# Kernel optimization log

Hardware: AMD Instinct MI355X
Metric: run time of the kernel (lower is better)

Reference implementation:

```python
import jax, jax.numpy as jnp
import numpy as np

HEADS = 12
D_HEAD = 64  # d_model // heads


def _split_heads(t, heads, d_head):
    # Faithful to the torch code: transpose(1,2) -> (B, C, T), then
    # reshape (B, -1, heads, d_head), then transpose(1,2) -> (B, heads, T', d_head).
    B = t.shape[0]
    t = jnp.swapaxes(t, 1, 2)                      # (B, C, T)
    t = t.reshape(B, -1, heads, d_head)            # (B, T', heads, d_head) -- layout quirk preserved
    return jnp.swapaxes(t, 1, 2)                   # (B, heads, T', d_head)


def setup_inputs() -> dict:
    key = jax.random.key(0)
    ks = jax.random.split(key, 10)
    B, Tq, Tkv, D = 8, 4096, 77, 768
    s = 0.02
    return {
        "x": jax.random.normal(ks[0], (B, Tq, D), jnp.float32),
        "prompt": jax.random.normal(ks[1], (B, Tkv, D), jnp.float32),
        "Wq": jax.random.normal(ks[2], (D, D), jnp.float32) * s,
        "bq": jax.random.normal(ks[3], (D,), jnp.float32) * s,
        "Wk": jax.random.normal(ks[4], (D, D), jnp.float32) * s,
        "bk": jax.random.normal(ks[5], (D,), jnp.float32) * s,
        "Wv": jax.random.normal(ks[6], (D, D), jnp.float32) * s,
        "bv": jax.random.normal(ks[7], (D,), jnp.float32) * s,
        "Wp": jax.random.normal(ks[8], (D, D), jnp.float32) * s,
        "bp": jax.random.normal(ks[9], (D,), jnp.float32) * s,
    }


def reference(x, prompt, Wq, bq, Wk, bk, Wv, bv, Wp, bp):
    B, Tq, C = x.shape
    Ckv = prompt.shape[-1]
    q = _split_heads(x @ Wq.T + bq, HEADS, D_HEAD)       # (B, H, Tq, d_head)
    k = _split_heads(prompt @ Wk.T + bk, HEADS, D_HEAD)  # (B, H, Tkv, d_head)
    v = _split_heads(prompt @ Wv.T + bv, HEADS, D_HEAD)
    scale = 1.0 / jnp.sqrt(jnp.asarray(Ckv, x.dtype))    # note: sqrt(d_prompt), as in source
    att = jnp.einsum('bhqd,bhkd->bhqk', q, k) * scale
    att = jax.nn.softmax(att, axis=-1)
    out = jnp.einsum('bhqk,bhkd->bhqd', att, v)          # (B, H, Tq, d_head)
    out = jnp.swapaxes(out, 1, 2).reshape(B, Tq, C)
    return out @ Wp.T + bp                               # dropout = identity (eval)
```

## Files before the change

kernel.cpp:

```cpp
#include <hip/hip_runtime.h>

typedef __attribute__((ext_vector_type(8))) __bf16 bf16x8;
typedef __attribute__((ext_vector_type(4))) float f32x4;
typedef __attribute__((ext_vector_type(8))) unsigned short u16x8;
typedef __attribute__((ext_vector_type(4))) unsigned short u16x4;

#define DEV __device__ __forceinline__

DEV float bf2f(unsigned short u) {
  unsigned int x = ((unsigned int)u) << 16;
  return __builtin_bit_cast(float, x);
}
DEV unsigned short f2bf(float f) {
  unsigned int u = __builtin_bit_cast(unsigned int, f);
  u = u + 0x7fffu + ((u >> 16) & 1u);
  return (unsigned short)(u >> 16);
}
DEV unsigned int cvtpk(float a, float b) {
  unsigned int r;
  asm("v_cvt_pk_bf16_f32 %0, %1, %2" : "=v"(r) : "v"(a), "v"(b));
  return r;
}

DEV void glds16(const void* g, void* l) {
  __builtin_amdgcn_global_load_lds(
      (__attribute__((address_space(1))) void*)g,
      (__attribute__((address_space(3))) void*)l, 16, 0, 0);
}

__global__ __launch_bounds__(256) void k_prep(
    const float* __restrict__ x, const float* __restrict__ Wq,
    const float* __restrict__ Wk, const float* __restrict__ Wv,
    const float* __restrict__ Wp, const float* __restrict__ prompt,
    const float* __restrict__ bk, const float* __restrict__ bv,
    unsigned short* __restrict__ xb, unsigned short* __restrict__ wqb,
    unsigned short* __restrict__ wkvb, unsigned short* __restrict__ wpb,
    unsigned short* __restrict__ pb, float* __restrict__ bkv,
    unsigned short* __restrict__ vt2) {
  const int blk = blockIdx.x;
  const int tid = threadIdx.x;
  if (blk < 2048) {
    for (int i = blk * 256 + tid; i < 6291456; i += 524288) {
      float4 v = reinterpret_cast<const float4*>(x)[i];
      u16x4 o;
      o[0] = f2bf(v.x); o[1] = f2bf(v.y); o[2] = f2bf(v.z); o[3] = f2bf(v.w);
      reinterpret_cast<u16x4*>(xb)[i] = o;
    }
  } else if (blk < 4352) {
    const int w = (blk - 2048) / 576;
    const int i = (blk - 2048 - w * 576) * 256 + tid;
    const float* src = (w == 0) ? Wq : (w == 1) ? Wk : (w == 2) ? Wv : Wp;
    unsigned short* dst =
        (w == 0) ? wqb : (w == 1) ? wkvb : (w == 2) ? (wkvb + 589824) : wpb;
    float4 v = reinterpret_cast<const float4*>(src)[i];
    u16x4 o;
    o[0] = f2bf(v.x); o[1] = f2bf(v.y); o[2] = f2bf(v.z); o[3] = f2bf(v.w);
    reinterpret_cast<u16x4*>(dst)[i] = o;
  } else if (blk < 5120) {
    const int i4 = (blk - 4352) * 256 + tid;
    const int e = i4 * 4;
    const int b = e / 98304;
    const int rem = e - b * 98304;
    const int s = rem / 768;
    const int d = rem - s * 768;
    u16x4 o;
    if (s < 77) {
      float4 v = *reinterpret_cast<const float4*>(&prompt[((long)b * 77 + s) * 768 + d]);
      o[0] = f2bf(v.x); o[1] = f2bf(v.y); o[2] = f2bf(v.z); o[3] = f2bf(v.w);
    } else {
      o[0] = 0; o[1] = 0; o[2] = 0; o[3] = 0;
    }
    reinterpret_cast<u16x4*>(pb)[i4] = o;
  } else if (blk < 5126) {
    const int i = (blk - 5120) * 256 + tid;
    if (i < 1536) bkv[i] = (i < 768) ? bk[i] : bv[i - 768];
  } else {
    const int i = (blk - 5126) * 256 + tid;
    u16x8 z = {};
    reinterpret_cast<u16x8*>(vt2)[i] = z;
  }
}

__global__ __launch_bounds__(256, 2) void k_qkv(
    const unsigned short* __restrict__ WQ, const unsigned short* __restrict__ XB,
    unsigned short* __restrict__ QT, const float* __restrict__ BQ,
    const unsigned short* __restrict__ WKV, const unsigned short* __restrict__ PB,
    unsigned short* __restrict__ KV, unsigned short* __restrict__ VT2,
    const float* __restrict__ BKV) {
  __shared__ alignas(16) unsigned short S[17408];
  unsigned short* const As = S;
  unsigned short* const Bs = S + 8192;

  const int tid = threadIdx.x;
  const int wave = tid >> 6;
  const int lane = tid & 63;
  const int wm = (wave >> 1) * 64;
  const int wn = (wave & 1) * 64;
  const int fr = lane & 15;
  const int fk = (lane >> 4) * 8;
  const int srow = lane >> 3;
  const int r0 = (lane >> 4) * 4;

  if (blockIdx.x >= 1536) {
    const int idx = blockIdx.x - 1536;
    const int bz = idx / 12;
    const int tm = (idx - bz * 12) * 128;
    const unsigned short* Bb = PB + (long)bz * 98304;
    const int scol = (lane & 7) * 8;

    f32x4 acc[4][4] = {};
    for (int k0 = 0; k0 < 768; k0 += 64) {
      __syncthreads();
#pragma unroll
      for (int i = 0; i < 4; ++i) {
        const int chunk = i * 4 + wave;
        glds16(WKV + (long)(tm + chunk * 8 + srow) * 768 + (k0 + scol), &As[chunk * 512]);
      }
#pragma unroll
      for (int i = 0; i < 4; ++i) {
        const int chunk = i * 4 + wave;
        glds16(Bb + (long)(chunk * 8 + srow) * 768 + (k0 + scol), &Bs[chunk * 512]);
      }
      __syncthreads();
#pragma unroll
      for (int ks = 0; ks < 2; ++ks) {
        bf16x8 af[4], bf[4];
#pragma unroll
        for (int mi = 0; mi < 4; ++mi)
          af[mi] = *reinterpret_cast<const bf16x8*>(&As[(wm + mi * 16 + fr) * 64 + ks * 32 + fk]);
#pragma unroll
        for (int ni = 0; ni < 4; ++ni)
          bf[ni] = *reinterpret_cast<const bf16x8*>(&Bs[(wn + ni * 16 + fr) * 64 + ks * 32 + fk]);
#pragma unroll
        for (int mi = 0; mi < 4; ++mi)
#pragma unroll
          for (int ni = 0; ni < 4; ++ni)
            acc[mi][ni] =
                __builtin_amdgcn_mfma_f32_16x16x32_bf16(af[mi], bf[ni], acc[mi][ni], 0, 0, 0);
      }
    }
#pragma unroll
    for (int mi = 0; mi < 4; ++mi) {
#pragma unroll
      for (int ni = 0; ni < 4; ++ni) {
        const int col = wn + ni * 16 + fr;
        if (col < 77) {
#pragma unroll
          for (int r = 0; r < 4; ++r) {
            const int row = tm + wm + mi * 16 + r0 + r;
            const unsigned short v = f2bf(acc[mi][ni][r] + BKV[row]);
            if (tm < 768) {
              KV[(long)bz * 59136 + (long)row * 77 + col] = v;
            } else {
              const int p = (row - 768) * 77 + col;
              const int snew = p / 768;
              const int c0 = p - snew * 768;
              VT2[(long)bz * 79872 + (long)c0 * 104 + snew] = v;
            }
          }
        }
      }
    }
    return;
  }

  const int l = (blockIdx.x & 7) * 192 + (blockIdx.x >> 3);
  const int tm = (l % 6) * 128;
  const int tn = (l / 6) * 128;
  const int srcx = ((lane & 7) ^ srow) * 8;
  const int rx = (fr & 7) * 8;

  f32x4 acc[4][4] = {};
  for (int k0 = 0; k0 < 768; k0 += 64) {
    __syncthreads();
#pragma unroll
    for (int i = 0; i < 4; ++i) {
      const int chunk = i * 4 + wave;
      glds16(WQ + (long)(tm + chunk * 8 + srow) * 768 + (k0 + srcx), &As[chunk * 512]);
    }
#pragma unroll
    for (int i = 0; i < 4; ++i) {
      const int chunk = i * 4 + wave;
      glds16(XB + (long)(tn + chunk * 8 + srow) * 768 + (k0 + srcx), &Bs[chunk * 512]);
    }
    __syncthreads();
#pragma unroll
    for (int ks = 0; ks < 2; ++ks) {
      bf16x8 af[4], bf[4];
#pragma unroll
      for (int mi = 0; mi < 4; ++mi)
        af[mi] = *reinterpret_cast<const bf16x8*>(
            &As[(wm + mi * 16 + fr) * 64 + ((ks * 32 + fk) ^ rx)]);
#pragma unroll
      for (int ni = 0; ni < 4; ++ni)
        bf[ni] = *reinterpret_cast<const bf16x8*>(
            &Bs[(wn + ni * 16 + fr) * 64 + ((ks * 32 + fk) ^ rx)]);
#pragma unroll
      for (int mi = 0; mi < 4; ++mi)
#pragma unroll
        for (int ni = 0; ni < 4; ++ni)
          acc[mi][ni] =
              __builtin_amdgcn_mfma_f32_16x16x32_bf16(af[mi], bf[ni], acc[mi][ni], 0, 0, 0);
    }
  }

  __syncthreads();
#pragma unroll
  for (int mi = 0; mi < 4; ++mi) {
    const int cmb = wm + mi * 16 + r0;
#pragma unroll
    for (int ni = 0; ni < 4; ++ni) {
      const int ct = wn + ni * 16 + fr;
      const unsigned int p01 =
          cvtpk(acc[mi][ni][0] + BQ[tm + cmb], acc[mi][ni][1] + BQ[tm + cmb + 1]);
      const unsigned int p23 =
          cvtpk(acc[mi][ni][2] + BQ[tm + cmb + 2], acc[mi][ni][3] + BQ[tm + cmb + 3]);
      S[(cmb + 0) * 136 + ct] = (unsigned short)p01;
      S[(cmb + 1) * 136 + ct] = (unsigned short)(p01 >> 16);
      S[(cmb + 2) * 136 + ct] = (unsigned short)p23;
      S[(cmb + 3) * 136 + ct] = (unsigned short)(p23 >> 16);
    }
  }
  __syncthreads();
  const int b_ = tn >> 12;
  const int toff = tn & 4095;
  const int cm = tid >> 1;
  const int t8 = (tid & 1) * 64;
  const long gb = (long)b_ * 3145728 + (long)(tm + cm) * 4096 + toff + t8;
#pragma unroll
  for (int j = 0; j < 8; ++j)
    *reinterpret_cast<u16x8*>(&QT[gb + j * 8]) =
        *reinterpret_cast<const u16x8*>(&S[cm * 136 + t8 + j * 8]);
}

__global__ __launch_bounds__(256, 2) void k_gout(const unsigned short* __restrict__ A,
                                                 const unsigned short* __restrict__ B,
                                                 float* __restrict__ out,
                                                 const float* __restrict__ bias) {
  __shared__ alignas(16) unsigned short S[16384];
  unsigned short* const As = S;
  unsigned short* const Bs = S + 8192;

  const int tid = threadIdx.x;
  const int wave = tid >> 6;
  const int lane = tid & 63;
  const int l = (blockIdx.x & 7) * 192 + (blockIdx.x >> 3);
  const int tm = (l / 6) * 128;
  const int tn = (l % 6) * 128;
  const int wm = (wave >> 1) * 64;
  const int wn = (wave & 1) * 64;
  const int fr = lane & 15;
  const int fk = (lane >> 4) * 8;
  const int srow = lane >> 3;
  const int srcx = ((lane & 7) ^ srow) * 8;
  const int rx = (fr & 7) * 8;

  f32x4 acc[4][4] = {};

  for (int k0 = 0; k0 < 768; k0 += 64) {
    __syncthreads();
#pragma unroll
    for (int i = 0; i < 4; ++i) {
      const int chunk = i * 4 + wave;
      glds16(A + (long)(tm + chunk * 8 + srow) * 768 + (k0 + srcx), &As[chunk * 512]);
    }
#pragma unroll
    for (int i = 0; i < 4; ++i) {
      const int chunk = i * 4 + wave;
      glds16(B + (long)(tn + chunk * 8 + srow) * 768 + (k0 + srcx), &Bs[chunk * 512]);
    }
    __syncthreads();
#pragma unroll
    for (int ks = 0; ks < 2; ++ks) {
      bf16x8 af[4], bf[4];
#pragma unroll
      for (int mi = 0; mi < 4; ++mi)
        af[mi] = *reinterpret_cast<const bf16x8*>(
            &As[(wm + mi * 16 + fr) * 64 + ((ks * 32 + fk) ^ rx)]);
#pragma unroll
      for (int ni = 0; ni < 4; ++ni)
        bf[ni] = *reinterpret_cast<const bf16x8*>(
            &Bs[(wn + ni * 16 + fr) * 64 + ((ks * 32 + fk) ^ rx)]);
#pragma unroll
      for (int mi = 0; mi < 4; ++mi)
#pragma unroll
        for (int ni = 0; ni < 4; ++ni)
          acc[mi][ni] =
              __builtin_amdgcn_mfma_f32_16x16x32_bf16(af[mi], bf[ni], acc[mi][ni], 0, 0, 0);
    }
  }

  const int r0 = (lane >> 4) * 4;
#pragma unroll
  for (int mi = 0; mi < 4; ++mi) {
#pragma unroll
    for (int ni = 0; ni < 4; ++ni) {
      const int col = tn + wn + ni * 16 + fr;
      const float bv = bias[col];
#pragma unroll
      for (int r = 0; r < 4; ++r) {
        const long g = tm + wm + mi * 16 + r0 + r;
        out[g * 768 + col] = acc[mi][ni][r] + bv;
      }
    }
  }
}

__global__ __launch_bounds__(256, 4) void k_attn(const unsigned short* __restrict__ QT,
                                                 const unsigned short* __restrict__ KVT,
                                                 const unsigned short* __restrict__ VT2,
                                                 unsigned short* __restrict__ Y) {
  __shared__ alignas(16) unsigned short Plds[128 * 104];
  __shared__ alignas(16) unsigned short Vt[64 * 104];

  const int b = blockIdx.z;
  const int h = blockIdx.y;
  const int tid = threadIdx.x;
  const int wave = tid >> 6;
  const int lane = tid & 63;
  const int fr = lane & 15;
  const int fg = lane >> 4;

  const unsigned short* vsrc = VT2 + (long)b * 79872 + h * 6656;
#pragma unroll
  for (int r = 0; r < 4; ++r) {
    const int chunk = r * 256 + tid;
    if (chunk < 832) glds16(vsrc + chunk * 8, &Vt[chunk * 8]);
  }

  {
    const int row = wave * 32 + (lane >> 1);
    u16x8 z = {};
    *reinterpret_cast<u16x8*>(&Plds[row * 104 + 80 + (lane & 1) * 8]) = z;
  }

  const int t0 = blockIdx.x * 128 + wave * 32;
  const long qb = (long)b * 3145728 + h * 64;
  const long kflat = (long)b * 59136 + h * 64;

  bf16x8 qa[2][2];
#pragma unroll
  for (int m = 0; m < 2; ++m)
#pragma unroll
    for (int ks = 0; ks < 2; ++ks)
      qa[m][ks] = *reinterpret_cast<const bf16x8*>(
          &QT[qb + (long)(t0 + m * 16 + fr) * 768 + ks * 32 + fg * 8]);

  bf16x8 kb[5][2];
#pragma unroll
  for (int n = 0; n < 5; ++n)
#pragma unroll
    for (int ks = 0; ks < 2; ++ks)
      kb[n][ks] = *reinterpret_cast<const bf16x8*>(
          &KVT[kflat + (long)(n * 16 + fr) * 768 + ks * 32 + fg * 8]);

  f32x4 s_[2][5] = {};
#pragma unroll
  for (int ks = 0; ks < 2; ++ks)
#pragma unroll
    for (int m = 0; m < 2; ++m)
#pragma unroll
      for (int n = 0; n < 5; ++n)
        s_[m][n] = __builtin_amdgcn_mfma_f32_16x16x32_bf16(qa[m][ks], kb[n][ks], s_[m][n], 0, 0, 0);

  const float scale = 0.036084391824351615f;
  f32x4 rl[2];
#pragma unroll
  for (int m = 0; m < 2; ++m) {
#pragma unroll
    for (int n = 0; n < 5; ++n) {
      const int key = n * 16 + fr;
#pragma unroll
      for (int r = 0; r < 4; ++r)
        s_[m][n][r] = (key < 77) ? __expf(s_[m][n][r] * scale) : 0.f;
    }
    f32x4 t = s_[m][0] + s_[m][1] + s_[m][2] + s_[m][3] + s_[m][4];
#pragma unroll
    for (int w = 1; w < 16; w <<= 1) {
      f32x4 u;
#pragma unroll
      for (int r = 0; r < 4; ++r) u[r] = __shfl_xor(t[r], w);
      t += u;
    }
    rl[m][0] = 1.f / t[0]; rl[m][1] = 1.f / t[1];
    rl[m][2] = 1.f / t[2]; rl[m][3] = 1.f / t[3];
  }

#pragma unroll
  for (int m = 0; m < 2; ++m)
#pragma unroll
    for (int n = 0; n < 5; ++n) {
      const unsigned int p01 = cvtpk(s_[m][n][0], s_[m][n][1]);
      const unsigned int p23 = cvtpk(s_[m][n][2], s_[m][n][3]);
      const int base = wave * 32 + m * 16 + fg * 4;
      const int col = n * 16 + fr;
      Plds[(base + 0) * 104 + col] = (unsigned short)p01;
      Plds[(base + 1) * 104 + col] = (unsigned short)(p01 >> 16);
      Plds[(base + 2) * 104 + col] = (unsigned short)p23;
      Plds[(base + 3) * 104 + col] = (unsigned short)(p23 >> 16);
    }

  __syncthreads();

  f32x4 o[2][4] = {};
#pragma unroll
  for (int ks = 0; ks < 3; ++ks) {
    bf16x8 pa[2], vb[4];
#pragma unroll
    for (int m = 0; m < 2; ++m)
      pa[m] = *reinterpret_cast<const bf16x8*>(
          &Plds[(wave * 32 + m * 16 + fr) * 104 + ks * 32 + fg * 8]);
#pragma unroll
    for (int n = 0; n < 4; ++n)
      vb[n] = *reinterpret_cast<const bf16x8*>(&Vt[(n * 16 + fr) * 104 + ks * 32 + fg * 8]);
#pragma unroll
    for (int m = 0; m < 2; ++m)
#pragma unroll
      for (int n = 0; n < 4; ++n)
        o[m][n] = __builtin_amdgcn_mfma_f32_16x16x32_bf16(pa[m], vb[n], o[m][n], 0, 0, 0);
  }

#pragma unroll
  for (int m = 0; m < 2; ++m)
#pragma unroll
    for (int n = 0; n < 4; ++n) {
      const unsigned int p01 = cvtpk(o[m][n][0] * rl[m][0], o[m][n][1] * rl[m][1]);
      const unsigned int p23 = cvtpk(o[m][n][2] * rl[m][2], o[m][n][3] * rl[m][3]);
      const int base = wave * 32 + m * 16 + fg * 4;
      const int col = n * 16 + fr;
      Plds[(base + 0) * 104 + col] = (unsigned short)p01;
      Plds[(base + 1) * 104 + col] = (unsigned short)(p01 >> 16);
      Plds[(base + 2) * 104 + col] = (unsigned short)p23;
      Plds[(base + 3) * 104 + col] = (unsigned short)(p23 >> 16);
    }
#pragma unroll
  for (int j = 0; j < 4; ++j) {
    const int chunk = j * 64 + lane;
    const int row = chunk >> 3;
    const int d8 = (chunk & 7) * 8;
    *reinterpret_cast<u16x8*>(&Y[qb + (long)(t0 + row) * 768 + d8]) =
        *reinterpret_cast<const u16x8*>(&Plds[(wave * 32 + row) * 104 + d8]);
  }
}

extern "C" void kernel_launch(void* const* d_in, const int* in_sizes, int n_in,
                              void* d_out, int out_size, void* d_ws, size_t ws_size,
                              hipStream_t stream) {
  const float* x      = (const float*)d_in[0];
  const float* prompt = (const float*)d_in[1];
  const float* Wq     = (const float*)d_in[2];
  const float* bq     = (const float*)d_in[3];
  const float* Wk     = (const float*)d_in[4];
  const float* bk     = (const float*)d_in[5];
  const float* Wv     = (const float*)d_in[6];
  const float* bv     = (const float*)d_in[7];
  const float* Wp     = (const float*)d_in[8];
  const float* bp     = (const float*)d_in[9];
  float* out = (float*)d_out;

  if (ws_size < 109185024u) return;
  char* ws = (char*)d_ws;
  unsigned short* xb   = (unsigned short*)(ws + 0);
  unsigned short* y    = xb;
  unsigned short* qt   = (unsigned short*)(ws + 50331648L);
  unsigned short* wqb  = (unsigned short*)(ws + 100663296L);
  unsigned short* wpb  = (unsigned short*)(ws + 101842944L);
  unsigned short* wkvb = (unsigned short*)(ws + 103022592L);
  unsigned short* pb   = (unsigned short*)(ws + 105381888L);
  unsigned short* kvt  = (unsigned short*)(ws + 106954752L);
  unsigned short* vt2  = (unsigned short*)(ws + 107900928L);
  float*          bkv  = (float*)(ws + 109178880L);

  k_prep<<<5438, 256, 0, stream>>>(x, Wq, Wk, Wv, Wp, prompt, bk, bv,
                                   xb, wqb, wkvb, wpb, pb, bkv, vt2);

  k_qkv<<<1632, 256, 0, stream>>>(wqb, xb, qt, bq, wkvb, pb, kvt, vt2, bkv);

  k_attn<<<dim3(32, 12, 8), 256, 0, stream>>>(qt, kvt, vt2, y);

  k_gout<<<1536, 256, 0, stream>>>(y, wpb, out, bp);
}
```

Baseline: 181.7 us.

## Fuse x fp32-to-bf16 conversion into Q projection GEMM tile loads

Drops the separate pass in the prep kernel that converted the large x activation to bf16. The Q-projection GEMM now streams fp32 x tiles directly into LDS with an XOR swizzle and converts them to bf16 with packed cvt while building MFMA fragments. This removes a full read and write of a 48MB buffer. In exchange it doubles the LDS bytes loaded for the B operand, raises shared memory per block to 48KB (which may limit occupancy), and adds conversion work inside the inner loop.

```diff
diff --git a/kernel.cpp b/kernel.cpp
--- a/kernel.cpp
+++ b/kernel.cpp
@@ -4,6 +4,7 @@
 typedef __attribute__((ext_vector_type(4))) float f32x4;
 typedef __attribute__((ext_vector_type(8))) unsigned short u16x8;
 typedef __attribute__((ext_vector_type(4))) unsigned short u16x4;
+typedef __attribute__((ext_vector_type(4))) unsigned int u32x4;
 
 #define DEV __device__ __forceinline__
 
@@ -29,26 +30,18 @@
 }
 
 __global__ __launch_bounds__(256) void k_prep(
-    const float* __restrict__ x, const float* __restrict__ Wq,
-    const float* __restrict__ Wk, const float* __restrict__ Wv,
-    const float* __restrict__ Wp, const float* __restrict__ prompt,
-    const float* __restrict__ bk, const float* __restrict__ bv,
-    unsigned short* __restrict__ xb, unsigned short* __restrict__ wqb,
-    unsigned short* __restrict__ wkvb, unsigned short* __restrict__ wpb,
-    unsigned short* __restrict__ pb, float* __restrict__ bkv,
-    unsigned short* __restrict__ vt2) {
+    const float* __restrict__ Wq, const float* __restrict__ Wk,
+    const float* __restrict__ Wv, const float* __restrict__ Wp,
+    const float* __restrict__ prompt, const float* __restrict__ bk,
+    const float* __restrict__ bv,
+    unsigned short* __restrict__ wqb, unsigned short* __restrict__ wkvb,
+    unsigned short* __restrict__ wpb, unsigned short* __restrict__ pb,
+    float* __restrict__ bkv, unsigned short* __restrict__ vt2) {
   const int blk = blockIdx.x;
   const int tid = threadIdx.x;
-  if (blk < 2048) {
-    for (int i = blk * 256 + tid; i < 6291456; i += 524288) {
-      float4 v = reinterpret_cast<const float4*>(x)[i];
-      u16x4 o;
-      o[0] = f2bf(v.x); o[1] = f2bf(v.y); o[2] = f2bf(v.z); o[3] = f2bf(v.w);
-      reinterpret_cast<u16x4*>(xb)[i] = o;
-    }
-  } else if (blk < 4352) {
-    const int w = (blk - 2048) / 576;
-    const int i = (blk - 2048 - w * 576) * 256 + tid;
+  if (blk < 2304) {
+    const int w = blk / 576;
+    const int i = (blk - w * 576) * 256 + tid;
     const float* src = (w == 0) ? Wq : (w == 1) ? Wk : (w == 2) ? Wv : Wp;
     unsigned short* dst =
         (w == 0) ? wqb : (w == 1) ? wkvb : (w == 2) ? (wkvb + 589824) : wpb;
@@ -56,8 +49,8 @@
     u16x4 o;
     o[0] = f2bf(v.x); o[1] = f2bf(v.y); o[2] = f2bf(v.z); o[3] = f2bf(v.w);
     reinterpret_cast<u16x4*>(dst)[i] = o;
-  } else if (blk < 5120) {
-    const int i4 = (blk - 4352) * 256 + tid;
+  } else if (blk < 3072) {
+    const int i4 = (blk - 2304) * 256 + tid;
     const int e = i4 * 4;
     const int b = e / 98304;
     const int rem = e - b * 98304;
@@ -71,25 +64,27 @@
       o[0] = 0; o[1] = 0; o[2] = 0; o[3] = 0;
     }
     reinterpret_cast<u16x4*>(pb)[i4] = o;
-  } else if (blk < 5126) {
-    const int i = (blk - 5120) * 256 + tid;
+  } else if (blk < 3078) {
+    const int i = (blk - 3072) * 256 + tid;
     if (i < 1536) bkv[i] = (i < 768) ? bk[i] : bv[i - 768];
   } else {
-    const int i = (blk - 5126) * 256 + tid;
+    const int i = (blk - 3078) * 256 + tid;
     u16x8 z = {};
     reinterpret_cast<u16x8*>(vt2)[i] = z;
   }
 }
 
 __global__ __launch_bounds__(256, 2) void k_qkv(
-    const unsigned short* __restrict__ WQ, const unsigned short* __restrict__ XB,
+    const unsigned short* __restrict__ WQ, const float* __restrict__ X,
     unsigned short* __restrict__ QT, const float* __restrict__ BQ,
     const unsigned short* __restrict__ WKV, const unsigned short* __restrict__ PB,
     unsigned short* __restrict__ KV, unsigned short* __restrict__ VT2,
     const float* __restrict__ BKV) {
-  __shared__ alignas(16) unsigned short S[17408];
-  unsigned short* const As = S;
-  unsigned short* const Bs = S + 8192;
+  __shared__ alignas(16) unsigned char SS[49152];
+  unsigned short* const As = (unsigned short*)SS;
+  unsigned short* const Bs = (unsigned short*)(SS + 16384);
+  float* const Bsf = (float*)(SS + 16384);
+  unsigned short* const S = (unsigned short*)SS;
 
   const int tid = threadIdx.x;
   const int wave = tid >> 6;
@@ -97,9 +92,10 @@
   const int wm = (wave >> 1) * 64;
   const int wn = (wave & 1) * 64;
   const int fr = lane & 15;
-  const int fk = (lane >> 4) * 8;
+  const int fg = lane >> 4;
+  const int fk = fg * 8;
   const int srow = lane >> 3;
-  const int r0 = (lane >> 4) * 4;
+  const int r0 = fg * 4;
 
   if (blockIdx.x >= 1536) {
     const int idx = blockIdx.x - 1536;
@@ -179,9 +175,11 @@
       glds16(WQ + (long)(tm + chunk * 8 + srow) * 768 + (k0 + srcx), &As[chunk * 512]);
     }
 #pragma unroll
-    for (int i = 0; i < 4; ++i) {
-      const int chunk = i * 4 + wave;
-      glds16(XB + (long)(tn + chunk * 8 + srow) * 768 + (k0 + srcx), &Bs[chunk * 512]);
+    for (int i = 0; i < 8; ++i) {
+      const int u = i * 4 + wave;
+      const int row = u * 4 + fg;
+      const int scol4 = ((lane & 15) ^ (row & 7)) * 4;
+      glds16(X + (long)(tn + row) * 768 + (k0 + scol4), Bsf + u * 256 + (lane & 15) * 4);
     }
     __syncthreads();
 #pragma unroll
@@ -192,9 +190,17 @@
         af[mi] = *reinterpret_cast<const bf16x8*>(
             &As[(wm + mi * 16 + fr) * 64 + ((ks * 32 + fk) ^ rx)]);
 #pragma unroll
-      for (int ni = 0; ni < 4; ++ni)
-        bf[ni] = *reinterpret_cast<const bf16x8*>(
-            &Bs[(wn + ni * 16 + fr) * 64 + ((ks * 32 + fk) ^ rx)]);
+      for (int ni = 0; ni < 4; ++ni) {
+        const int rb = wn + ni * 16 + fr;
+        const int r7 = fr & 7;
+        const int sb0 = ks * 8 + fg * 2;
+        f32x4 lo = *reinterpret_cast<const f32x4*>(&Bsf[rb * 64 + ((sb0 ^ r7) * 4)]);
+        f32x4 hi = *reinterpret_cast<const f32x4*>(&Bsf[rb * 64 + (((sb0 | 1) ^ r7) * 4)]);
+        u32x4 w;
+        w[0] = cvtpk(lo[0], lo[1]); w[1] = cvtpk(lo[2], lo[3]);
+        w[2] = cvtpk(hi[0], hi[1]); w[3] = cvtpk(hi[2], hi[3]);
+        bf[ni] = __builtin_bit_cast(bf16x8, w);
+      }
 #pragma unroll
       for (int mi = 0; mi < 4; ++mi)
 #pragma unroll
@@ -460,8 +466,7 @@
 
   if (ws_size < 109185024u) return;
   char* ws = (char*)d_ws;
-  unsigned short* xb   = (unsigned short*)(ws + 0);
-  unsigned short* y    = xb;
+  unsigned short* y    = (unsigned short*)(ws + 0);
   unsigned short* qt   = (unsigned short*)(ws + 50331648L);
   unsigned short* wqb  = (unsigned short*)(ws + 100663296L);
   unsigned short* wpb  = (unsigned short*)(ws + 101842944L);
@@ -471,10 +476,10 @@
   unsigned short* vt2  = (unsigned short*)(ws + 107900928L);
   float*          bkv  = (float*)(ws + 109178880L);
 
-  k_prep<<<5438, 256, 0, stream>>>(x, Wq, Wk, Wv, Wp, prompt, bk, bv,
-                                   xb, wqb, wkvb, wpb, pb, bkv, vt2);
-
-  k_qkv<<<1632, 256, 0, stream>>>(wqb, xb, qt, bq, wkvb, pb, kvt, vt2, bkv);
+  k_prep<<<3390, 256, 0, stream>>>(Wq, Wk, Wv, Wp, prompt, bk, bv,
+                                   wqb, wkvb, wpb, pb, bkv, vt2);
+
+  k_qkv<<<1632, 256, 0, stream>>>(wqb, x, qt, bq, wkvb, pb, kvt, vt2, bkv);
 
   k_attn<<<dim3(32, 12, 8), 256, 0, stream>>>(qt, kvt, vt2, y);
 
```

Result: no change. 184.1 us (+1.3%).
